# Kernel optimization log

Measured on AMD Instinct MI355X. Metric: run time of the kernel, lower is better.

Reference implementation:

```python
import jax, jax.numpy as jnp
import numpy as np

N_NODES = 50000
N_EDGES = 800000
FEATURES = 64
HIDDEN = 128
OUT_DIM = 64
CUTOFF = 10.0
STEP = 0.1
N_MU = 100  # len(arange(0, 10, 0.1))


def setup_inputs() -> dict:
    key = jax.random.key(0)
    k_h, k_src, k_dst, k_norm, k_w1, k_w2 = jax.random.split(key, 6)
    h = jax.random.normal(k_h, (N_NODES, FEATURES), dtype=jnp.float32)
    src = jax.random.randint(k_src, (N_EDGES,), 0, N_NODES, dtype=jnp.int64)
    dst = jax.random.randint(k_dst, (N_EDGES,), 0, N_NODES, dtype=jnp.int64)
    edge_norm = jax.random.uniform(k_norm, (N_EDGES,), dtype=jnp.float32) * CUTOFF
    mu = jnp.arange(0.0, CUTOFF, STEP, dtype=jnp.float32)  # [100], learned param
    in_dim = 2 * FEATURES + N_MU
    # xavier_normal with gain split across 2 linear layers: layer_gain = 1.0
    s1 = float(np.sqrt(2.0 / (in_dim + HIDDEN)))
    s2 = float(np.sqrt(2.0 / (HIDDEN + OUT_DIM)))
    W1 = jax.random.normal(k_w1, (HIDDEN, in_dim), dtype=jnp.float32) * s1
    W2 = jax.random.normal(k_w2, (OUT_DIM, HIDDEN), dtype=jnp.float32) * s2
    return {"h": h, "src": src, "dst": dst, "edge_norm": edge_norm,
            "mu": mu, "W1": W1, "W2": W2}


def reference(h, src, dst, edge_norm, mu, W1, W2):
    # Gaussian RBF expansion of edge distances: [E, n_mu]
    d_emb = jnp.exp((-1.0 / STEP) * (mu[None, :] - edge_norm[:, None]) ** 2)
    # gather endpoint features and concat: [E, 2*features + n_mu]
    x = jnp.concatenate((h[src], h[dst], d_emb), axis=-1)
    # MLP: Linear(no bias) -> SiLU -> Linear(no bias)
    hdn = jax.nn.silu(x @ W1.T)
    return hdn @ W2.T
```

## Files before the change

### kernel.cpp

```cpp
#include <hip/hip_runtime.h>
#include <hip/hip_bf16.h>


#define FEAT     64
#define NMU      100
#define K1_REAL  228
#define HID      128
#define ODIM     64
#define K2       128
#define WEDGES   32
#define NWAVES   16
#define BEDGES   (WEDGES * NWAVES)
#define LDH2     136
#define HROWS    16
#define HN8      400000

typedef __bf16 bf16x8 __attribute__((ext_vector_type(8)));
typedef float  fx4    __attribute__((ext_vector_type(4)));

__global__ void pack_w(const float* __restrict__ W1, const float* __restrict__ W2,
                       __bf16* __restrict__ B1, __bf16* __restrict__ B2) {
    int i = blockIdx.x * 256 + threadIdx.x;
    if (i < 32768) {
        int j  = i & 7;
        int n  = (i >> 3) & 127;
        int qk = i >> 10;
        int k  = (qk >> 2) * 32 + (qk & 3) * 8 + j;
        float v = (k < K1_REAL) ? W1[n * K1_REAL + k] : 0.0f;
        B1[i] = (__bf16)v;
    } else {
        int t = i - 32768;
        int j  = t & 7;
        int n  = (t >> 3) & 63;
        int qk = t >> 9;
        int k  = (qk >> 2) * 32 + (qk & 3) * 8 + j;
        B2[t] = (__bf16)W2[n * K2 + k];
    }
}

__global__ void pack_h(const float* __restrict__ h, __bf16* __restrict__ hb) {
    int i = blockIdx.x * 256 + threadIdx.x;
    if (i >= HN8) return;
    const float4* p = (const float4*)h + (size_t)i * 2;
    float4 v0 = p[0];
    float4 v1 = p[1];
    bf16x8 b = { (__bf16)v0.x, (__bf16)v0.y, (__bf16)v0.z, (__bf16)v0.w,
                 (__bf16)v1.x, (__bf16)v1.y, (__bf16)v1.z, (__bf16)v1.w };
    ((bf16x8*)hb)[i] = b;
}

__device__ __forceinline__ bf16x8 hfrag_f32(const float* __restrict__ h, int node, int cb) {
    const float4* p = (const float4*)(h + (size_t)node * FEAT + cb);
    float4 v0 = p[0];
    float4 v1 = p[1];
    bf16x8 a = { (__bf16)v0.x, (__bf16)v0.y, (__bf16)v0.z, (__bf16)v0.w,
                 (__bf16)v1.x, (__bf16)v1.y, (__bf16)v1.z, (__bf16)v1.w };
    return a;
}

template<bool HB16>
__global__ __launch_bounds__(1024, 4)
void edges_fused(const float* __restrict__ h,
                 const __bf16* __restrict__ hb,
                 const int*   __restrict__ src,
                 const int*   __restrict__ dst,
                 const float* __restrict__ enorm,
                 const float* __restrict__ mu,
                 const __bf16* __restrict__ B1,
                 const __bf16* __restrict__ B2,
                 float* __restrict__ out,
                 int E) {
    __shared__ __bf16 B1s[32768];
    __shared__ __bf16 B2s[8192];
    __shared__ __bf16 Hs[NWAVES * HROWS * LDH2];

    const int tid  = threadIdx.x;
    const int w    = tid >> 6;
    const int lane = tid & 63;
    const int ln   = lane & 15;
    const int q    = lane >> 4;
    const int g0   = blockIdx.x * BEDGES + w * WEDGES;
    const bool act = (g0 < E);

    int nsrc[2], ndst[2];
    float dval[2];
    bf16x8 ag[4][2];
    if (act) {
#pragma unroll
        for (int mt = 0; mt < 2; ++mt) {
            int e = g0 + mt * 16 + ln;
            nsrc[mt] = src[e];
            ndst[mt] = dst[e];
            dval[mt] = enorm[e];
        }
#pragma unroll
        for (int kk = 0; kk < 4; ++kk) {
            const int cb = (kk & 1) * 32 + q * 8;
#pragma unroll
            for (int mt = 0; mt < 2; ++mt) {
                int node = (kk < 2) ? nsrc[mt] : ndst[mt];
                if constexpr (HB16)
                    ag[kk][mt] = *(const bf16x8*)(hb + (size_t)node * FEAT + cb);
                else
                    ag[kk][mt] = hfrag_f32(h, node, cb);
            }
        }
    }

    {
        const bf16x8* gB1 = (const bf16x8*)B1;
        const bf16x8* gB2 = (const bf16x8*)B2;
        bf16x8* sB1 = (bf16x8*)B1s;
        bf16x8* sB2 = (bf16x8*)B2s;
#pragma unroll
        for (int it = 0; it < 4; ++it) {
            int g = it * 1024 + tid;
            sB1[g] = gB1[g];
        }
        sB2[tid] = gB2[tid];
    }
    __syncthreads();
    if (!act) return;

    fx4 acc1[2][8];
#pragma unroll
    for (int mt = 0; mt < 2; ++mt)
#pragma unroll
        for (int nt = 0; nt < 8; ++nt)
            acc1[mt][nt] = (fx4){0.f, 0.f, 0.f, 0.f};

#pragma unroll
    for (int kk = 4; kk < 7; ++kk) {
        const int c0 = (kk - 4) * 32 + q * 8;
        float4 m0 = *(const float4*)(mu + c0);
        float4 m1 = *(const float4*)(mu + c0 + 4);
        bf16x8 a[2];
#pragma unroll
        for (int mt = 0; mt < 2; ++mt) {
            float d = dval[mt];
            float t0 = m0.x - d, t1 = m0.y - d, t2 = m0.z - d, t3 = m0.w - d;
            float t4 = m1.x - d, t5 = m1.y - d, t6 = m1.z - d, t7 = m1.w - d;
            a[mt] = (bf16x8){ (__bf16)__expf(-10.f * t0 * t0), (__bf16)__expf(-10.f * t1 * t1),
                              (__bf16)__expf(-10.f * t2 * t2), (__bf16)__expf(-10.f * t3 * t3),
                              (__bf16)__expf(-10.f * t4 * t4), (__bf16)__expf(-10.f * t5 * t5),
                              (__bf16)__expf(-10.f * t6 * t6), (__bf16)__expf(-10.f * t7 * t7) };
        }
#pragma unroll
        for (int nt = 0; nt < 8; ++nt) {
            bf16x8 b = *(const bf16x8*)&B1s[(((kk * 4 + q) * 128) + nt * 16 + ln) * 8];
            acc1[0][nt] = __builtin_amdgcn_mfma_f32_16x16x32_bf16(a[0], b, acc1[0][nt], 0, 0, 0);
            acc1[1][nt] = __builtin_amdgcn_mfma_f32_16x16x32_bf16(a[1], b, acc1[1][nt], 0, 0, 0);
        }
    }
    {
        float4 m7 = *(const float4*)(mu + 96);
        const __bf16 zz = (__bf16)0.0f;
        const bool qz = (q == 0);
        bf16x8 a[2];
#pragma unroll
        for (int mt = 0; mt < 2; ++mt) {
            float d = dval[mt];
            float t0 = m7.x - d, t1 = m7.y - d, t2 = m7.z - d, t3 = m7.w - d;
            a[mt] = (bf16x8){ qz ? (__bf16)__expf(-10.f * t0 * t0) : zz,
                              qz ? (__bf16)__expf(-10.f * t1 * t1) : zz,
                              qz ? (__bf16)__expf(-10.f * t2 * t2) : zz,
                              qz ? (__bf16)__expf(-10.f * t3 * t3) : zz,
                              zz, zz, zz, zz };
        }
#pragma unroll
        for (int nt = 0; nt < 8; ++nt) {
            bf16x8 b = *(const bf16x8*)&B1s[(((7 * 4 + q) * 128) + nt * 16 + ln) * 8];
            acc1[0][nt] = __builtin_amdgcn_mfma_f32_16x16x32_bf16(a[0], b, acc1[0][nt], 0, 0, 0);
            acc1[1][nt] = __builtin_amdgcn_mfma_f32_16x16x32_bf16(a[1], b, acc1[1][nt], 0, 0, 0);
        }
    }
#pragma unroll
    for (int kk = 0; kk < 4; ++kk) {
#pragma unroll
        for (int nt = 0; nt < 8; ++nt) {
            bf16x8 b = *(const bf16x8*)&B1s[(((kk * 4 + q) * 128) + nt * 16 + ln) * 8];
            acc1[0][nt] = __builtin_amdgcn_mfma_f32_16x16x32_bf16(ag[kk][0], b, acc1[0][nt], 0, 0, 0);
            acc1[1][nt] = __builtin_amdgcn_mfma_f32_16x16x32_bf16(ag[kk][1], b, acc1[1][nt], 0, 0, 0);
        }
    }

    __bf16* Hw = &Hs[w * HROWS * LDH2];
#pragma unroll
    for (int mt = 0; mt < 2; ++mt) {
#pragma unroll
        for (int nt = 0; nt < 8; ++nt)
#pragma unroll
            for (int r = 0; r < 4; ++r) {
                float z = acc1[mt][nt][r];
                float s = z * __builtin_amdgcn_rcpf(1.0f + __expf(-z));
                Hw[(q * 4 + r) * LDH2 + nt * 16 + ln] = (__bf16)s;
            }

        fx4 acc2[4];
#pragma unroll
        for (int nt = 0; nt < 4; ++nt)
            acc2[nt] = (fx4){0.f, 0.f, 0.f, 0.f};
#pragma unroll
        for (int kk = 0; kk < 4; ++kk) {
            bf16x8 a2 = *(const bf16x8*)&Hw[ln * LDH2 + kk * 32 + q * 8];
#pragma unroll
            for (int nt = 0; nt < 4; ++nt) {
                bf16x8 b2 = *(const bf16x8*)&B2s[(((kk * 4 + q) * 64) + nt * 16 + ln) * 8];
                acc2[nt] = __builtin_amdgcn_mfma_f32_16x16x32_bf16(a2, b2, acc2[nt], 0, 0, 0);
            }
        }

#pragma unroll
        for (int nt = 0; nt < 4; ++nt)
#pragma unroll
            for (int r = 0; r < 4; ++r)
                out[(size_t)(g0 + mt * 16 + q * 4 + r) * ODIM + nt * 16 + ln] = acc2[nt][r];
    }
}

extern "C" void kernel_launch(void* const* d_in, const int* in_sizes, int n_in,
                              void* d_out, int out_size, void* d_ws, size_t ws_size,
                              hipStream_t stream) {
    const float* h   = (const float*)d_in[0];
    const int*   src = (const int*)d_in[1];
    const int*   dst = (const int*)d_in[2];
    const float* en  = (const float*)d_in[3];
    const float* mu  = (const float*)d_in[4];
    const float* W1  = (const float*)d_in[5];
    const float* W2  = (const float*)d_in[6];

    __bf16* B1 = (__bf16*)d_ws;
    __bf16* B2 = (__bf16*)((char*)d_ws + 65536);
    __bf16* HB = (__bf16*)((char*)d_ws + 81920);

    const size_t ws_needed = 81920 + (size_t)HN8 * 8 * sizeof(__bf16);
    const bool   use_hb    = ws_size >= ws_needed;

    pack_w<<<160, 256, 0, stream>>>(W1, W2, B1, B2);

    const int E = in_sizes[1];
    const int nblocks = (E + BEDGES - 1) / BEDGES;

    if (use_hb) {
        pack_h<<<(HN8 + 255) / 256, 256, 0, stream>>>(h, HB);
        edges_fused<true><<<nblocks, 1024, 0, stream>>>(h, HB, src, dst, en, mu, B1, B2, (float*)d_out, E);
    } else {
        edges_fused<false><<<nblocks, 1024, 0, stream>>>(h, nullptr, src, dst, en, mu, B1, B2, (float*)d_out, E);
    }
}
```

Before: 324.4 us.

## Switch edge MLP to 32x32x16 MFMA with register-resident hidden layer

```diff
diff --git a/kernel.cpp b/kernel.cpp
--- a/kernel.cpp
+++ b/kernel.cpp
@@ -2,39 +2,37 @@
 #include <hip/hip_bf16.h>
 
 
-#define FEAT     64
-#define NMU      100
-#define K1_REAL  228
-#define HID      128
-#define ODIM     64
-#define K2       128
-#define WEDGES   32
-#define NWAVES   16
-#define BEDGES   (WEDGES * NWAVES)
-#define LDH2     136
-#define HROWS    16
-#define HN8      400000
-
-typedef __bf16 bf16x8 __attribute__((ext_vector_type(8)));
-typedef float  fx4    __attribute__((ext_vector_type(4)));
+#define FEAT      64
+#define NMU       100
+#define K1_REAL   228
+#define WEDGES    32
+#define NWAVES    8
+#define BEDGES    (WEDGES * NWAVES)
+#define HN8       400000
+#define B1N_ELEMS 30720
+#define B2N_ELEMS 8192
+
+typedef __bf16  bf16x8 __attribute__((ext_vector_type(8)));
+typedef float   fx16   __attribute__((ext_vector_type(16)));
 
 __global__ void pack_w(const float* __restrict__ W1, const float* __restrict__ W2,
                        __bf16* __restrict__ B1, __bf16* __restrict__ B2) {
     int i = blockIdx.x * 256 + threadIdx.x;
-    if (i < 32768) {
-        int j  = i & 7;
-        int n  = (i >> 3) & 127;
-        int qk = i >> 10;
-        int k  = (qk >> 2) * 32 + (qk & 3) * 8 + j;
+    if (i < B1N_ELEMS) {
+        int j   = i & 7;
+        int n   = (i >> 3) & 127;
+        int ksh = i >> 10;
+        int k   = ksh * 8 + j;
         float v = (k < K1_REAL) ? W1[n * K1_REAL + k] : 0.0f;
         B1[i] = (__bf16)v;
-    } else {
-        int t = i - 32768;
-        int j  = t & 7;
-        int n  = (t >> 3) & 63;
-        int qk = t >> 9;
-        int k  = (qk >> 2) * 32 + (qk & 3) * 8 + j;
-        B2[t] = (__bf16)W2[n * K2 + k];
+    } else if (i < B1N_ELEMS + B2N_ELEMS) {
+        int t   = i - B1N_ELEMS;
+        int j   = t & 7;
+        int n2  = (t >> 3) & 63;
+        int sh  = t >> 9;
+        int rho = ((sh >> 2) << 5) | (((sh >> 1) & 1) << 4)
+                | ((j >> 2) << 3) | ((sh & 1) << 2) | (j & 3);
+        B2[t] = (__bf16)W2[n2 * 128 + rho];
     }
 }
 
@@ -58,8 +56,18 @@
     return a;
 }
 
+__device__ __forceinline__ float silu(float z) {
+    return z * __builtin_amdgcn_rcpf(1.0f + __expf(-z));
+}
+
+__device__ __forceinline__ uint32_t pkbf16(float x, float y) {
+    union { __bf16 b; uint16_t u; } cx, cy;
+    cx.b = (__bf16)x; cy.b = (__bf16)y;
+    return (uint32_t)cx.u | ((uint32_t)cy.u << 16);
+}
+
 template<bool HB16>
-__global__ __launch_bounds__(1024, 4)
+__global__ __launch_bounds__(512, 4)
 void edges_fused(const float* __restrict__ h,
                  const __bf16* __restrict__ hb,
                  const int*   __restrict__ src,
@@ -70,40 +78,31 @@
                  const __bf16* __restrict__ B2,
                  float* __restrict__ out,
                  int E) {
-    __shared__ __bf16 B1s[32768];
-    __shared__ __bf16 B2s[8192];
-    __shared__ __bf16 Hs[NWAVES * HROWS * LDH2];
-
-    const int tid  = threadIdx.x;
-    const int w    = tid >> 6;
-    const int lane = tid & 63;
-    const int ln   = lane & 15;
-    const int q    = lane >> 4;
-    const int g0   = blockIdx.x * BEDGES + w * WEDGES;
+    __shared__ __align__(16) __bf16 B1s[B1N_ELEMS];
+    __shared__ __align__(16) __bf16 B2s[B2N_ELEMS];
+
+    const int tid = threadIdx.x;
+    const int w   = tid >> 6;
+    const int m   = tid & 31;
+    const int h5  = (tid >> 5) & 1;
+    const int g0  = blockIdx.x * BEDGES + w * WEDGES;
     const bool act = (g0 < E);
 
-    int nsrc[2], ndst[2];
-    float dval[2];
-    bf16x8 ag[4][2];
+    int ndst;
+    float dval;
+    bf16x8 ags[4];
     if (act) {
-#pragma unroll
-        for (int mt = 0; mt < 2; ++mt) {
-            int e = g0 + mt * 16 + ln;
-            nsrc[mt] = src[e];
-            ndst[mt] = dst[e];
-            dval[mt] = enorm[e];
-        }
-#pragma unroll
-        for (int kk = 0; kk < 4; ++kk) {
-            const int cb = (kk & 1) * 32 + q * 8;
-#pragma unroll
-            for (int mt = 0; mt < 2; ++mt) {
-                int node = (kk < 2) ? nsrc[mt] : ndst[mt];
-                if constexpr (HB16)
-                    ag[kk][mt] = *(const bf16x8*)(hb + (size_t)node * FEAT + cb);
-                else
-                    ag[kk][mt] = hfrag_f32(h, node, cb);
-            }
+        int e = g0 + m;
+        int nsrc = src[e];
+        ndst = dst[e];
+        dval = enorm[e];
+#pragma unroll
+        for (int ks = 0; ks < 4; ++ks) {
+            const int cb = ks * 16 + h5 * 8;
+            if constexpr (HB16)
+                ags[ks] = *(const bf16x8*)(hb + (size_t)nsrc * FEAT + cb);
+            else
+                ags[ks] = hfrag_f32(h, nsrc, cb);
         }
     }
 
@@ -113,109 +112,116 @@
         bf16x8* sB1 = (bf16x8*)B1s;
         bf16x8* sB2 = (bf16x8*)B2s;
 #pragma unroll
-        for (int it = 0; it < 4; ++it) {
-            int g = it * 1024 + tid;
-            sB1[g] = gB1[g];
-        }
-        sB2[tid] = gB2[tid];
+        for (int it = 0; it < 8; ++it) {
+            int g = it * 512 + tid;
+            if (g < B1N_ELEMS / 8) sB1[g] = gB1[g];
+        }
+#pragma unroll
+        for (int it = 0; it < 2; ++it) {
+            int g = it * 512 + tid;
+            sB2[g] = gB2[g];
+        }
     }
     __syncthreads();
     if (!act) return;
 
-    fx4 acc1[2][8];
-#pragma unroll
-    for (int mt = 0; mt < 2; ++mt)
-#pragma unroll
-        for (int nt = 0; nt < 8; ++nt)
-            acc1[mt][nt] = (fx4){0.f, 0.f, 0.f, 0.f};
-
-#pragma unroll
-    for (int kk = 4; kk < 7; ++kk) {
-        const int c0 = (kk - 4) * 32 + q * 8;
+    fx16 acc1[4] = {};
+
+#pragma unroll
+    for (int ks = 8; ks < 14; ++ks) {
+        const int c0 = ks * 16 - 128 + h5 * 8;
         float4 m0 = *(const float4*)(mu + c0);
         float4 m1 = *(const float4*)(mu + c0 + 4);
-        bf16x8 a[2];
-#pragma unroll
-        for (int mt = 0; mt < 2; ++mt) {
-            float d = dval[mt];
-            float t0 = m0.x - d, t1 = m0.y - d, t2 = m0.z - d, t3 = m0.w - d;
-            float t4 = m1.x - d, t5 = m1.y - d, t6 = m1.z - d, t7 = m1.w - d;
-            a[mt] = (bf16x8){ (__bf16)__expf(-10.f * t0 * t0), (__bf16)__expf(-10.f * t1 * t1),
-                              (__bf16)__expf(-10.f * t2 * t2), (__bf16)__expf(-10.f * t3 * t3),
-                              (__bf16)__expf(-10.f * t4 * t4), (__bf16)__expf(-10.f * t5 * t5),
-                              (__bf16)__expf(-10.f * t6 * t6), (__bf16)__expf(-10.f * t7 * t7) };
-        }
-#pragma unroll
-        for (int nt = 0; nt < 8; ++nt) {
-            bf16x8 b = *(const bf16x8*)&B1s[(((kk * 4 + q) * 128) + nt * 16 + ln) * 8];
-            acc1[0][nt] = __builtin_amdgcn_mfma_f32_16x16x32_bf16(a[0], b, acc1[0][nt], 0, 0, 0);
-            acc1[1][nt] = __builtin_amdgcn_mfma_f32_16x16x32_bf16(a[1], b, acc1[1][nt], 0, 0, 0);
+        const float d = dval;
+        float t0 = m0.x - d, t1 = m0.y - d, t2 = m0.z - d, t3 = m0.w - d;
+        float t4 = m1.x - d, t5 = m1.y - d, t6 = m1.z - d, t7 = m1.w - d;
+        bf16x8 a = { (__bf16)__expf(-10.f * t0 * t0), (__bf16)__expf(-10.f * t1 * t1),
+                     (__bf16)__expf(-10.f * t2 * t2), (__bf16)__expf(-10.f * t3 * t3),
+                     (__bf16)__expf(-10.f * t4 * t4), (__bf16)__expf(-10.f * t5 * t5),
+                     (__bf16)__expf(-10.f * t6 * t6), (__bf16)__expf(-10.f * t7 * t7) };
+        const int base = ((ks * 2 + h5) * 128 + m) * 8;
+#pragma unroll
+        for (int nt1 = 0; nt1 < 4; ++nt1) {
+            bf16x8 a1 = *(const bf16x8*)&B1s[base + nt1 * 256];
+            acc1[nt1] = __builtin_amdgcn_mfma_f32_32x32x16_bf16(a1, a, acc1[nt1], 0, 0, 0);
         }
     }
     {
         float4 m7 = *(const float4*)(mu + 96);
+        const float d = dval;
+        const bool lo = (h5 == 0);
         const __bf16 zz = (__bf16)0.0f;
-        const bool qz = (q == 0);
-        bf16x8 a[2];
-#pragma unroll
-        for (int mt = 0; mt < 2; ++mt) {
-            float d = dval[mt];
-            float t0 = m7.x - d, t1 = m7.y - d, t2 = m7.z - d, t3 = m7.w - d;
-            a[mt] = (bf16x8){ qz ? (__bf16)__expf(-10.f * t0 * t0) : zz,
-                              qz ? (__bf16)__expf(-10.f * t1 * t1) : zz,
-                              qz ? (__bf16)__expf(-10.f * t2 * t2) : zz,
-                              qz ? (__bf16)__expf(-10.f * t3 * t3) : zz,
-                              zz, zz, zz, zz };
-        }
-#pragma unroll
-        for (int nt = 0; nt < 8; ++nt) {
-            bf16x8 b = *(const bf16x8*)&B1s[(((7 * 4 + q) * 128) + nt * 16 + ln) * 8];
-            acc1[0][nt] = __builtin_amdgcn_mfma_f32_16x16x32_bf16(a[0], b, acc1[0][nt], 0, 0, 0);
-            acc1[1][nt] = __builtin_amdgcn_mfma_f32_16x16x32_bf16(a[1], b, acc1[1][nt], 0, 0, 0);
-        }
-    }
-#pragma unroll
-    for (int kk = 0; kk < 4; ++kk) {
-#pragma unroll
-        for (int nt = 0; nt < 8; ++nt) {
-            bf16x8 b = *(const bf16x8*)&B1s[(((kk * 4 + q) * 128) + nt * 16 + ln) * 8];
-            acc1[0][nt] = __builtin_amdgcn_mfma_f32_16x16x32_bf16(ag[kk][0], b, acc1[0][nt], 0, 0, 0);
-            acc1[1][nt] = __builtin_amdgcn_mfma_f32_16x16x32_bf16(ag[kk][1], b, acc1[1][nt], 0, 0, 0);
-        }
-    }
-
-    __bf16* Hw = &Hs[w * HROWS * LDH2];
-#pragma unroll
-    for (int mt = 0; mt < 2; ++mt) {
-#pragma unroll
-        for (int nt = 0; nt < 8; ++nt)
-#pragma unroll
-            for (int r = 0; r < 4; ++r) {
-                float z = acc1[mt][nt][r];
-                float s = z * __builtin_amdgcn_rcpf(1.0f + __expf(-z));
-                Hw[(q * 4 + r) * LDH2 + nt * 16 + ln] = (__bf16)s;
+        float t0 = m7.x - d, t1 = m7.y - d, t2 = m7.z - d, t3 = m7.w - d;
+        bf16x8 a = { lo ? (__bf16)__expf(-10.f * t0 * t0) : zz,
+                     lo ? (__bf16)__expf(-10.f * t1 * t1) : zz,
+                     lo ? (__bf16)__expf(-10.f * t2 * t2) : zz,
+                     lo ? (__bf16)__expf(-10.f * t3 * t3) : zz,
+                     zz, zz, zz, zz };
+        const int base = ((14 * 2 + h5) * 128 + m) * 8;
+#pragma unroll
+        for (int nt1 = 0; nt1 < 4; ++nt1) {
+            bf16x8 a1 = *(const bf16x8*)&B1s[base + nt1 * 256];
+            acc1[nt1] = __builtin_amdgcn_mfma_f32_32x32x16_bf16(a1, a, acc1[nt1], 0, 0, 0);
+        }
+    }
+#pragma unroll
+    for (int ks = 0; ks < 4; ++ks) {
+        const int base = ((ks * 2 + h5) * 128 + m) * 8;
+#pragma unroll
+        for (int nt1 = 0; nt1 < 4; ++nt1) {
+            bf16x8 a1 = *(const bf16x8*)&B1s[base + nt1 * 256];
+            acc1[nt1] = __builtin_amdgcn_mfma_f32_32x32x16_bf16(a1, ags[ks], acc1[nt1], 0, 0, 0);
+        }
+    }
+#pragma unroll
+    for (int ks = 0; ks < 4; ++ks) {
+        const int cb = ks * 16 + h5 * 8;
+        if constexpr (HB16)
+            ags[ks] = *(const bf16x8*)(hb + (size_t)ndst * FEAT + cb);
+        else
+            ags[ks] = hfrag_f32(h, ndst, cb);
+    }
+#pragma unroll
+    for (int ks = 4; ks < 8; ++ks) {
+        const int base = ((ks * 2 + h5) * 128 + m) * 8;
+#pragma unroll
+        for (int nt1 = 0; nt1 < 4; ++nt1) {
+            bf16x8 a1 = *(const bf16x8*)&B1s[base + nt1 * 256];
+            acc1[nt1] = __builtin_amdgcn_mfma_f32_32x32x16_bf16(a1, ags[ks - 4], acc1[nt1], 0, 0, 0);
+        }
+    }
+
+    fx16 acc2[2] = {};
+#pragma unroll
+    for (int nt1 = 0; nt1 < 4; ++nt1) {
+        uint32_t P[8];
+#pragma unroll
+        for (int gp = 0; gp < 8; ++gp)
+            P[gp] = pkbf16(silu(acc1[nt1][2 * gp]), silu(acc1[nt1][2 * gp + 1]));
+#pragma unroll
+        for (int t = 0; t < 2; ++t) {
+            const int s = nt1 * 2 + t;
+            union { uint32_t u[4]; bf16x8 v; } uu;
+            uu.u[0] = P[4 * t + 0]; uu.u[1] = P[4 * t + 1];
+            uu.u[2] = P[4 * t + 2]; uu.u[3] = P[4 * t + 3];
+            const int base2 = ((s * 2 + h5) * 64 + m) * 8;
+#pragma unroll
+            for (int n2t = 0; n2t < 2; ++n2t) {
+                bf16x8 a2 = *(const bf16x8*)&B2s[base2 + n2t * 256];
+                acc2[n2t] = __builtin_amdgcn_mfma_f32_32x32x16_bf16(a2, uu.v, acc2[n2t], 0, 0, 0);
             }
-
-        fx4 acc2[4];
-#pragma unroll
-        for (int nt = 0; nt < 4; ++nt)
-            acc2[nt] = (fx4){0.f, 0.f, 0.f, 0.f};
-#pragma unroll
-        for (int kk = 0; kk < 4; ++kk) {
-            bf16x8 a2 = *(const bf16x8*)&Hw[ln * LDH2 + kk * 32 + q * 8];
-#pragma unroll
-            for (int nt = 0; nt < 4; ++nt) {
-                bf16x8 b2 = *(const bf16x8*)&B2s[(((kk * 4 + q) * 64) + nt * 16 + ln) * 8];
-                acc2[nt] = __builtin_amdgcn_mfma_f32_16x16x32_bf16(a2, b2, acc2[nt], 0, 0, 0);
-            }
-        }
-
-#pragma unroll
-        for (int nt = 0; nt < 4; ++nt)
-#pragma unroll
-            for (int r = 0; r < 4; ++r)
-                out[(size_t)(g0 + mt * 16 + q * 4 + r) * ODIM + nt * 16 + ln] = acc2[nt][r];
-    }
+        }
+    }
+
+    float* orow = out + (size_t)(g0 + m) * 64 + h5 * 4;
+#pragma unroll
+    for (int n2t = 0; n2t < 2; ++n2t)
+#pragma unroll
+        for (int g = 0; g < 4; ++g) {
+            float4 st = { acc2[n2t][4 * g + 0], acc2[n2t][4 * g + 1],
+                          acc2[n2t][4 * g + 2], acc2[n2t][4 * g + 3] };
+            *(float4*)(orow + n2t * 32 + g * 8) = st;
+        }
 }
 
 extern "C" void kernel_launch(void* const* d_in, const int* in_sizes, int n_in,
@@ -230,21 +236,21 @@
     const float* W2  = (const float*)d_in[6];
 
     __bf16* B1 = (__bf16*)d_ws;
-    __bf16* B2 = (__bf16*)((char*)d_ws + 65536);
-    __bf16* HB = (__bf16*)((char*)d_ws + 81920);
-
-    const size_t ws_needed = 81920 + (size_t)HN8 * 8 * sizeof(__bf16);
+    __bf16* B2 = (__bf16*)((char*)d_ws + 61440);
+    __bf16* HB = (__bf16*)((char*)d_ws + 77824);
+
+    const size_t ws_needed = 77824 + (size_t)HN8 * 8 * sizeof(__bf16);
     const bool   use_hb    = ws_size >= ws_needed;
 
-    pack_w<<<160, 256, 0, stream>>>(W1, W2, B1, B2);
+    pack_w<<<(B1N_ELEMS + B2N_ELEMS) / 256, 256, 0, stream>>>(W1, W2, B1, B2);
 
     const int E = in_sizes[1];
     const int nblocks = (E + BEDGES - 1) / BEDGES;
 
     if (use_hb) {
         pack_h<<<(HN8 + 255) / 256, 256, 0, stream>>>(h, HB);
-        edges_fused<true><<<nblocks, 1024, 0, stream>>>(h, HB, src, dst, en, mu, B1, B2, (float*)d_out, E);
+        edges_fused<true><<<nblocks, 512, 0, stream>>>(h, HB, src, dst, en, mu, B1, B2, (float*)d_out, E);
     } else {
-        edges_fused<false><<<nblocks, 1024, 0, stream>>>(h, nullptr, src, dst, en, mu, B1, B2, (float*)d_out, E);
-    }
-}
+        edges_fused<false><<<nblocks, 512, 0, stream>>>(h, nullptr, src, dst, en, mu, B1, B2, (float*)d_out, E);
+    }
+}
```

After: 303.9 us. -6.3%, faster.
